# Optimization experiments

Measured on AMD Instinct MI355X. Metric: run time of the kernel, lower is better.

The kernel has to match this reference:

```python
import jax, jax.numpy as jnp
import numpy as np

EPS = 1e-06  # slot-attention renorm epsilon
LN_EPS = 1e-05  # torch LayerNorm default
NUM_ITERS = 3


def layernorm(x, w, b):
    m = jnp.mean(x, axis=-1, keepdims=True)
    v = jnp.mean((x - m) ** 2, axis=-1, keepdims=True)
    return (x - m) * jax.lax.rsqrt(v + LN_EPS) * w + b


def setup_inputs() -> dict:
    key = jax.random.key(0)
    ks = jax.random.split(key, 16)
    B, N, D = 32, 4096, 512
    S, NS, H = 128, 8, 256
    def lin(k, out_f, in_f):
        return jax.random.normal(k, (out_f, in_f), jnp.float32) * (1.0 / np.sqrt(in_f))
    return {
        "inputs": jax.random.normal(ks[0], (B, N, D), jnp.float32),
        "slots_init": jax.random.normal(ks[1], (B, NS, S), jnp.float32),
        "ln_in_w": jnp.ones((D,), jnp.float32), "ln_in_b": jnp.zeros((D,), jnp.float32),
        "ln_slot_w": jnp.ones((S,), jnp.float32), "ln_slot_b": jnp.zeros((S,), jnp.float32),
        "ln_mlp_w": jnp.ones((S,), jnp.float32), "ln_mlp_b": jnp.zeros((S,), jnp.float32),
        "Wq": lin(ks[2], S, S), "Wk": lin(ks[3], S, D), "Wv": lin(ks[4], S, D),
        "gru_Wih": lin(ks[5], 3 * S, S), "gru_Whh": lin(ks[6], 3 * S, S),
        "gru_bih": jnp.zeros((3 * S,), jnp.float32), "gru_bhh": jnp.zeros((3 * S,), jnp.float32),
        "mlp_W1": lin(ks[7], H, S), "mlp_b1": jnp.zeros((H,), jnp.float32),
        "mlp_W2": lin(ks[8], S, H), "mlp_b2": jnp.zeros((S,), jnp.float32),
        "slots_mu": jax.random.normal(ks[9], (1, 1, S), jnp.float32) * 0.1,
        "slots_log_sigma": jax.random.normal(ks[10], (1, 1, S), jnp.float32) * 0.1,
    }


def gru_cell(x, h, Wih, Whh, bih, bhh):
    # PyTorch GRUCell math. x, h: [BS, S]
    S = h.shape[-1]
    gi = x @ Wih.T + bih
    gh = h @ Whh.T + bhh
    i_r, i_z, i_n = gi[:, :S], gi[:, S:2 * S], gi[:, 2 * S:]
    h_r, h_z, h_n = gh[:, :S], gh[:, S:2 * S], gh[:, 2 * S:]
    r = jax.nn.sigmoid(i_r + h_r)
    z = jax.nn.sigmoid(i_z + h_z)
    n = jnp.tanh(i_n + r * h_n)
    return (1.0 - z) * n + z * h


def reference(inputs, slots_init, ln_in_w, ln_in_b, ln_slot_w, ln_slot_b, ln_mlp_w, ln_mlp_b,
              Wq, Wk, Wv, gru_Wih, gru_Whh, gru_bih, gru_bhh,
              mlp_W1, mlp_b1, mlp_W2, mlp_b2, slots_mu, slots_log_sigma):
    B, N, D = inputs.shape
    NS, S = slots_init.shape[1], slots_init.shape[2]
    x = layernorm(inputs, ln_in_w, ln_in_b)
    k = jnp.einsum('bnd,sd->bns', x, Wk)  # [B,N,S]
    v = jnp.einsum('bnd,sd->bns', x, Wv)
    slots = slots_mu + jnp.exp(slots_log_sigma) * slots_init  # [B,NS,S]
    scale = S ** (-0.5)
    for _ in range(NUM_ITERS):
        slots_prev = slots
        q = jnp.einsum('bmd,sd->bms', layernorm(slots, ln_slot_w, ln_slot_b), Wq)  # [B,NS,S]
        attn_logits = scale * jnp.einsum('bns,bms->bnm', k, q)  # [B,N,NS]
        attn = jax.nn.softmax(attn_logits, axis=-1) + EPS
        attn = attn / jnp.sum(attn, axis=1, keepdims=True)  # normalize over inputs
        updates = jnp.einsum('bnm,bns->bms', attn, v)  # [B,NS,S]
        h = gru_cell(updates.reshape(B * NS, S), slots_prev.reshape(B * NS, S),
                     gru_Wih, gru_Whh, gru_bih, gru_bhh).reshape(B, NS, S)
        mlp_out = jnp.maximum(layernorm(h, ln_mlp_w, ln_mlp_b) @ mlp_W1.T + mlp_b1, 0.0) @ mlp_W2.T + mlp_b2
        slots = h + mlp_out
    return slots
```

## Files before the change

### kernel.cpp

```cpp
#include <hip/hip_runtime.h>

typedef __bf16 v8bf __attribute__((ext_vector_type(8)));
typedef __bf16 v4bf __attribute__((ext_vector_type(4)));
typedef float  v4f  __attribute__((ext_vector_type(4)));
typedef unsigned short u16;

#define LN_EPS_F 1e-5f
#define ATTN_EPS 1e-6f

static constexpr int Bsz = 32;
static constexpr int Nn  = 4096;
static constexpr int Dd  = 512;
static constexpr int Ss  = 128;
static constexpr int NSs = 8;
static constexpr int Hh  = 256;
static constexpr int MROWS = Bsz * Nn;

__device__ __forceinline__ void load_lds16(const void* g, void* l) {
    __builtin_amdgcn_global_load_lds(
        (const __attribute__((address_space(1))) void*)g,
        (__attribute__((address_space(3))) void*)l, 16, 0, 0);
}

__global__ __launch_bounds__(256) void k_prep(const float* __restrict__ Wk, const float* __restrict__ Wv,
                                              const float* __restrict__ ln_in_w, const float* __restrict__ ln_in_b,
                                              const float* __restrict__ slots_init, const float* __restrict__ mu,
                                              const float* __restrict__ lsig,
                                              u16* __restrict__ Wkvp, float* __restrict__ cb,
                                              float* __restrict__ Scol, float* __restrict__ slots) {
    const int bid = blockIdx.x;
    const int t = threadIdx.x;
    if (bid < 512) {
        int idx = bid * 256 + t;
        int n = idx >> 9, d = idx & 511;
        float w = (n < Ss) ? Wk[n * Dd + d] : Wv[(n - Ss) * Dd + d];
        w *= ln_in_w[d];
        __bf16 bv = (__bf16)w;
        Wkvp[idx] = __builtin_bit_cast(u16, bv);
    } else if (bid < 640) {
        int idx = (bid - 512) * 256 + t;
        int sidx = idx & (Ss - 1);
        slots[idx] = mu[sidx] + expf(lsig[sidx]) * slots_init[idx];
    } else {
        const float* wrow = (t < Ss) ? (Wk + t * Dd) : (Wv + (t - Ss) * Dd);
        float accb = 0.f, accs = 0.f;
        for (int d = 0; d < Dd; ++d) {
            float w  = wrow[d];
            float wb = (float)(__bf16)(w * ln_in_w[d]);
            accs += wb;
            accb += ln_in_b[d] * w;
        }
        cb[t]   = accb;
        Scol[t] = accs;
    }
}

__global__ __launch_bounds__(256) void k_kvgemm(const float* __restrict__ X,
                                                const u16* __restrict__ Wkvp,
                                                const float* __restrict__ cb,
                                                const float* __restrict__ Scol,
                                                u16* __restrict__ kv) {
    __shared__ __bf16 As[64][72];
    __shared__ __bf16 Bs[256 * 64];
    __shared__ float2 stats_sh[64];
    const int t    = threadIdx.x;
    const int lane = t & 63;
    const int wid  = t >> 6;
    const size_t m0 = (size_t)blockIdx.x * 64;

    const int ar  = t >> 2;
    const int ac0 = (t & 3) * 16;
    const float* xrow = X + (m0 + ar) * Dd;

    const int sub  = lane >> 3;
    const int scol = ((lane & 7) ^ sub) * 8;
    const u16* bsrc = Wkvp + (size_t)(wid * 64 + sub) * Dd + scol;

    const v4f vzero = {0.f, 0.f, 0.f, 0.f};
    v4f acc[4][4];
#pragma unroll
    for (int i = 0; i < 4; ++i)
#pragma unroll
        for (int j = 0; j < 4; ++j) acc[i][j] = vzero;

    const int g  = lane >> 4;
    const int lr = lane & 15;
    float s1 = 0.f, s2 = 0.f;

    for (int kb = 0; kb < 8; ++kb) {
#pragma unroll
        for (int p = 0; p < 8; ++p)
            load_lds16(bsrc + (size_t)p * 8 * Dd + kb * 64,
                       &Bs[(wid * 64 + p * 8) * 64]);
#pragma unroll
        for (int j = 0; j < 4; ++j) {
            float4 xv = *reinterpret_cast<const float4*>(xrow + kb * 64 + ac0 + j * 4);
            s1 += xv.x + xv.y + xv.z + xv.w;
            s2 += xv.x * xv.x + xv.y * xv.y + xv.z * xv.z + xv.w * xv.w;
            v4bf wv;
            wv[0] = (__bf16)xv.x; wv[1] = (__bf16)xv.y;
            wv[2] = (__bf16)xv.z; wv[3] = (__bf16)xv.w;
            *reinterpret_cast<v4bf*>(&As[ar][ac0 + j * 4]) = wv;
        }
        __syncthreads();
#pragma unroll
        for (int ks = 0; ks < 2; ++ks) {
            v8bf a[4], b[4];
#pragma unroll
            for (int mi = 0; mi < 4; ++mi)
                a[mi] = *reinterpret_cast<const v8bf*>(&As[mi * 16 + lr][ks * 32 + g * 8]);
#pragma unroll
            for (int ni = 0; ni < 4; ++ni) {
                int r = wid * 64 + ni * 16 + lr;
                b[ni] = *reinterpret_cast<const v8bf*>(
                    &Bs[r * 64 + ((ks * 32 + g * 8) ^ ((lr & 7) * 8))]);
            }
#pragma unroll
            for (int mi = 0; mi < 4; ++mi)
#pragma unroll
                for (int ni = 0; ni < 4; ++ni)
                    acc[mi][ni] = __builtin_amdgcn_mfma_f32_16x16x32_bf16(a[mi], b[ni], acc[mi][ni], 0, 0, 0);
        }
        __syncthreads();
    }
    s1 += __shfl_xor(s1, 1); s1 += __shfl_xor(s1, 2);
    s2 += __shfl_xor(s2, 1); s2 += __shfl_xor(s2, 2);
    if ((t & 3) == 0) {
        float m = s1 * (1.f / Dd);
        float v = s2 * (1.f / Dd) - m * m;
        stats_sh[ar] = make_float2(m, rsqrtf(v + LN_EPS_F));
    }
    __syncthreads();
    float Sn[4], cbv[4];
#pragma unroll
    for (int ni = 0; ni < 4; ++ni) {
        int ng = wid * 64 + ni * 16 + lr;
        Sn[ni]  = Scol[ng];
        cbv[ni] = cb[ng];
    }
#pragma unroll
    for (int mi = 0; mi < 4; ++mi)
#pragma unroll
        for (int j = 0; j < 4; ++j) {
            float2 st = stats_sh[mi * 16 + g * 4 + j];
            size_t mg = m0 + mi * 16 + g * 4 + j;
#pragma unroll
            for (int ni = 0; ni < 4; ++ni) {
                int ng = wid * 64 + ni * 16 + lr;
                float val = st.y * (acc[mi][ni][j] - st.x * Sn[ni]) + cbv[ni];
                __bf16 bv = (__bf16)val;
                kv[mg * 256 + ng] = __builtin_bit_cast(u16, bv);
            }
        }
}

__global__ __launch_bounds__(128) void k_q(const float* __restrict__ slots,
                                           const float* __restrict__ lnw, const float* __restrict__ lnb,
                                           const float* __restrict__ Wq, float* __restrict__ q) {
    __shared__ float xs[128];
    __shared__ float red[4];
    const int t = threadIdx.x;
    const int bm = blockIdx.x;
    float x = slots[bm * 128 + t];
    float s = x, s2 = x * x;
#pragma unroll
    for (int off = 32; off > 0; off >>= 1) { s += __shfl_xor(s, off); s2 += __shfl_xor(s2, off); }
    const int wid = t >> 6, lane = t & 63;
    if (lane == 0) { red[wid * 2] = s; red[wid * 2 + 1] = s2; }
    __syncthreads();
    float S1 = red[0] + red[2], S2 = red[1] + red[3];
    float m = S1 * (1.f / 128.f);
    float rstd = rsqrtf(S2 * (1.f / 128.f) - m * m + LN_EPS_F);
    xs[t] = (x - m) * rstd * lnw[t] + lnb[t];
    __syncthreads();
    const float* wr = Wq + (size_t)t * 128;
    float acc = 0.f;
#pragma unroll 8
    for (int d = 0; d < 128; d += 4) {
        float4 w = *reinterpret_cast<const float4*>(wr + d);
        acc += w.x * xs[d] + w.y * xs[d + 1] + w.z * xs[d + 2] + w.w * xs[d + 3];
    }
    q[bm * 128 + t] = acc * 0.08838834764831845f;
}

__global__ __launch_bounds__(256) void k_attnupd(const u16* __restrict__ kv, const float* __restrict__ q,
                                                 float* __restrict__ upd_part, float* __restrict__ colsum_part) {
    __shared__ float qs[8 * 128];
    __shared__ float at[128][8];
    __shared__ __bf16 vt[128][128];
    __shared__ float colpart[4][8];
    const int b  = blockIdx.y;
    const int ch = blockIdx.x;
    const int t  = threadIdx.x;
    const int lane = t & 63, wv = t >> 6;
    *reinterpret_cast<float4*>(&qs[t * 4]) = *reinterpret_cast<const float4*>(&q[b * 1024 + t * 4]);
    __syncthreads();
    {
        const int rsub = lane >> 4;
        const int csub = (lane & 15) * 8;
#pragma unroll
        for (int p = 0; p < 8; ++p) {
            int row = wv * 32 + p * 4;
            const u16* src = kv + ((size_t)(b * Nn + ch * 128 + row + rsub)) * 256 + 128 + csub;
            load_lds16(src, &vt[row][0]);
        }
    }
    const int nl   = t >> 1;
    const int half = t & 1;
    const u16* krow = kv + ((size_t)(b * Nn + ch * 128 + nl)) * 256 + half * 64;
    float acc[8] = {0.f, 0.f, 0.f, 0.f, 0.f, 0.f, 0.f, 0.f};
#pragma unroll
    for (int c = 0; c < 8; ++c) {
        v8bf kvv = *reinterpret_cast<const v8bf*>(krow + c * 8);
        float kf[8];
#pragma unroll
        for (int j = 0; j < 8; ++j) kf[j] = (float)kvv[j];
#pragma unroll
        for (int m = 0; m < 8; ++m) {
            const float* qrow = &qs[m * 128 + half * 64 + c * 8];
            float aa = 0.f;
#pragma unroll
            for (int j = 0; j < 8; ++j) aa += kf[j] * qrow[j];
            acc[m] += aa;
        }
    }
#pragma unroll
    for (int m = 0; m < 8; ++m) acc[m] += __shfl_xor(acc[m], 1);
    float mx = acc[0];
#pragma unroll
    for (int m = 1; m < 8; ++m) mx = fmaxf(mx, acc[m]);
    float e[8]; float ssum = 0.f;
#pragma unroll
    for (int m = 0; m < 8; ++m) { e[m] = __expf(acc[m] - mx); ssum += e[m]; }
    float inv = 1.0f / ssum;
    float a8[8];
#pragma unroll
    for (int m = 0; m < 8; ++m) a8[m] = e[m] * inv + ATTN_EPS;
    *reinterpret_cast<float4*>(&at[nl][half * 4]) =
        make_float4(a8[half * 4], a8[half * 4 + 1], a8[half * 4 + 2], a8[half * 4 + 3]);
#pragma unroll
    for (int m = 0; m < 8; ++m) {
        float v = a8[m];
#pragma unroll
        for (int off = 32; off > 0; off >>= 1) v += __shfl_xor(v, off);
        if (lane == 0) colpart[wv][m] = v * 0.5f;
    }
    __syncthreads();
    const int m2 = t >> 5;
    const int s0 = (t & 31) * 4;
    float a0 = 0.f, a1 = 0.f, a2 = 0.f, a3 = 0.f;
#pragma unroll 4
    for (int n = 0; n < 128; ++n) {
        float a = at[n][m2];
        v4bf vvv = *reinterpret_cast<const v4bf*>(&vt[n][s0]);
        a0 += a * (float)vvv[0];
        a1 += a * (float)vvv[1];
        a2 += a * (float)vvv[2];
        a3 += a * (float)vvv[3];
    }
    *reinterpret_cast<float4*>(upd_part + ((size_t)(b * 32 + ch) * 8 + m2) * 128 + s0) =
        make_float4(a0, a1, a2, a3);
    if (t < 8)
        colsum_part[(b * 32 + ch) * 8 + t] =
            colpart[0][t] + colpart[1][t] + colpart[2][t] + colpart[3][t];
}

__global__ __launch_bounds__(128) void k_finishq(const float* __restrict__ upd_part,
                                                 const float* __restrict__ colsum_part,
                                                 const float* __restrict__ slots_in,
                                                 const float* __restrict__ Wih, const float* __restrict__ Whh,
                                                 const float* __restrict__ bih, const float* __restrict__ bhh,
                                                 const float* __restrict__ lnw, const float* __restrict__ lnb,
                                                 const float* __restrict__ W1, const float* __restrict__ b1,
                                                 const float* __restrict__ W2, const float* __restrict__ b2,
                                                 const float* __restrict__ lnsw, const float* __restrict__ lnsb,
                                                 const float* __restrict__ Wq,
                                                 float* __restrict__ slots_out, float* __restrict__ qout) {
    __shared__ float us[128], sp[128], hnorm[128], act[256];
    __shared__ float red[4];
    __shared__ float csum_sh;
    const int t  = threadIdx.x;
    const int bm = blockIdx.x;
    const int b = bm >> 3, m = bm & 7;
    if (t < 64) {
        float v = (t < 32) ? colsum_part[(b * 32 + t) * 8 + m] : 0.f;
#pragma unroll
        for (int off = 32; off > 0; off >>= 1) v += __shfl_xor(v, off);
        if (t == 0) csum_sh = v;
    }
    float u = 0.f;
    for (int chk = 0; chk < 32; ++chk)
        u += upd_part[((size_t)(b * 32 + chk) * 8 + m) * 128 + t];
    float h0 = slots_in[bm * 128 + t];
    sp[t] = h0;
    __syncthreads();
    u *= (1.0f / csum_sh);
    us[t] = u;
    __syncthreads();
    float gir = bih[t], giz = bih[Ss + t], gin = bih[2 * Ss + t];
    float ghr = bhh[t], ghz = bhh[Ss + t], ghn = bhh[2 * Ss + t];
#pragma unroll 4
    for (int d = 0; d < Ss; d += 4) {
        float u0 = us[d], u1 = us[d + 1], u2 = us[d + 2], u3 = us[d + 3];
        float p0 = sp[d], p1 = sp[d + 1], p2 = sp[d + 2], p3 = sp[d + 3];
        float4 w;
        w = *reinterpret_cast<const float4*>(Wih + (size_t)t * Ss + d);
        gir += w.x * u0 + w.y * u1 + w.z * u2 + w.w * u3;
        w = *reinterpret_cast<const float4*>(Wih + (size_t)(Ss + t) * Ss + d);
        giz += w.x * u0 + w.y * u1 + w.z * u2 + w.w * u3;
        w = *reinterpret_cast<const float4*>(Wih + (size_t)(2 * Ss + t) * Ss + d);
        gin += w.x * u0 + w.y * u1 + w.z * u2 + w.w * u3;
        w = *reinterpret_cast<const float4*>(Whh + (size_t)t * Ss + d);
        ghr += w.x * p0 + w.y * p1 + w.z * p2 + w.w * p3;
        w = *reinterpret_cast<const float4*>(Whh + (size_t)(Ss + t) * Ss + d);
        ghz += w.x * p0 + w.y * p1 + w.z * p2 + w.w * p3;
        w = *reinterpret_cast<const float4*>(Whh + (size_t)(2 * Ss + t) * Ss + d);
        ghn += w.x * p0 + w.y * p1 + w.z * p2 + w.w * p3;
    }
    float r  = 1.f / (1.f + __expf(-(gir + ghr)));
    float z  = 1.f / (1.f + __expf(-(giz + ghz)));
    float nn = tanhf(gin + r * ghn);
    float h  = (1.f - z) * nn + z * h0;
    float s = h, s2 = h * h;
#pragma unroll
    for (int off = 32; off > 0; off >>= 1) { s += __shfl_xor(s, off); s2 += __shfl_xor(s2, off); }
    const int lane = t & 63, w2 = t >> 6;
    if (lane == 0) { red[w2 * 2] = s; red[w2 * 2 + 1] = s2; }
    __syncthreads();
    float S1 = red[0] + red[2], S2 = red[1] + red[3];
    float mean = S1 * (1.f / Ss);
    float rstd = rsqrtf(S2 * (1.f / Ss) - mean * mean + LN_EPS_F);
    hnorm[t] = (h - mean) * rstd * lnw[t] + lnb[t];
    __syncthreads();
    float a1 = b1[t], a2 = b1[Ss + t];
#pragma unroll 4
    for (int d = 0; d < Ss; d += 4) {
        float h0_ = hnorm[d], h1_ = hnorm[d + 1], h2_ = hnorm[d + 2], h3_ = hnorm[d + 3];
        float4 w1v = *reinterpret_cast<const float4*>(W1 + (size_t)t * Ss + d);
        float4 w2v = *reinterpret_cast<const float4*>(W1 + (size_t)(Ss + t) * Ss + d);
        a1 += w1v.x * h0_ + w1v.y * h1_ + w1v.z * h2_ + w1v.w * h3_;
        a2 += w2v.x * h0_ + w2v.y * h1_ + w2v.z * h2_ + w2v.w * h3_;
    }
    act[t] = fmaxf(a1, 0.f);
    act[Ss + t] = fmaxf(a2, 0.f);
    __syncthreads();
    float o = b2[t];
#pragma unroll 4
    for (int j = 0; j < Hh; j += 4) {
        float4 wv = *reinterpret_cast<const float4*>(W2 + (size_t)t * Hh + j);
        o += wv.x * act[j] + wv.y * act[j + 1] + wv.z * act[j + 2] + wv.w * act[j + 3];
    }
    float snew = h + o;
    slots_out[bm * 128 + t] = snew;
    float ss1 = snew, ss2 = snew * snew;
#pragma unroll
    for (int off = 32; off > 0; off >>= 1) { ss1 += __shfl_xor(ss1, off); ss2 += __shfl_xor(ss2, off); }
    if (lane == 0) { red[w2 * 2] = ss1; red[w2 * 2 + 1] = ss2; }
    __syncthreads();
    float T1 = red[0] + red[2], T2 = red[1] + red[3];
    float m2 = T1 * (1.f / Ss);
    float rstd2 = rsqrtf(T2 * (1.f / Ss) - m2 * m2 + LN_EPS_F);
    hnorm[t] = (snew - m2) * rstd2 * lnsw[t] + lnsb[t];
    __syncthreads();
    const float* wr = Wq + (size_t)t * 128;
    float qa = 0.f;
#pragma unroll 8
    for (int d = 0; d < 128; d += 4) {
        float4 w = *reinterpret_cast<const float4*>(wr + d);
        qa += w.x * hnorm[d] + w.y * hnorm[d + 1] + w.z * hnorm[d + 2] + w.w * hnorm[d + 3];
    }
    qout[bm * 128 + t] = qa * 0.08838834764831845f;
}

extern "C" void kernel_launch(void* const* d_in, const int* in_sizes, int n_in,
                              void* d_out, int out_size, void* d_ws, size_t ws_size,
                              hipStream_t stream) {
    const float* X          = (const float*)d_in[0];
    const float* slots_init = (const float*)d_in[1];
    const float* ln_in_w    = (const float*)d_in[2];
    const float* ln_in_b    = (const float*)d_in[3];
    const float* ln_slot_w  = (const float*)d_in[4];
    const float* ln_slot_b  = (const float*)d_in[5];
    const float* ln_mlp_w   = (const float*)d_in[6];
    const float* ln_mlp_b   = (const float*)d_in[7];
    const float* Wq         = (const float*)d_in[8];
    const float* Wk         = (const float*)d_in[9];
    const float* Wv         = (const float*)d_in[10];
    const float* gWih       = (const float*)d_in[11];
    const float* gWhh       = (const float*)d_in[12];
    const float* gbih       = (const float*)d_in[13];
    const float* gbhh       = (const float*)d_in[14];
    const float* W1         = (const float*)d_in[15];
    const float* b1         = (const float*)d_in[16];
    const float* W2         = (const float*)d_in[17];
    const float* b2         = (const float*)d_in[18];
    const float* mu         = (const float*)d_in[19];
    const float* lsig       = (const float*)d_in[20];

    char* p = (char*)d_ws;
    u16*    Wkvp        = (u16*)p;    p += (size_t)256 * 512 * sizeof(u16);
    float*  cb          = (float*)p;  p += 256 * sizeof(float);
    float*  Scol        = (float*)p;  p += 256 * sizeof(float);
    float*  slots       = (float*)p;  p += 32 * 8 * 128 * sizeof(float);
    float*  qbuf        = (float*)p;  p += 32 * 8 * 128 * sizeof(float);
    float*  colsum_part = (float*)p;  p += 32 * 32 * 8 * sizeof(float);
    float*  upd_part    = (float*)p;  p += (size_t)32 * 32 * 8 * 128 * sizeof(float);
    u16*    kv          = (u16*)p;    p += (size_t)MROWS * 256 * sizeof(u16);

    k_prep<<<641, 256, 0, stream>>>(Wk, Wv, ln_in_w, ln_in_b, slots_init, mu, lsig,
                                    Wkvp, cb, Scol, slots);
    k_kvgemm<<<MROWS / 64, 256, 0, stream>>>(X, Wkvp, cb, Scol, kv);
    k_q<<<256, 128, 0, stream>>>(slots, ln_slot_w, ln_slot_b, Wq, qbuf);

    for (int it = 0; it < 3; ++it) {
        k_attnupd<<<dim3(32, 32), 256, 0, stream>>>(kv, qbuf, upd_part, colsum_part);
        k_finishq<<<256, 128, 0, stream>>>(upd_part, colsum_part, slots,
                                           gWih, gWhh, gbih, gbhh,
                                           ln_mlp_w, ln_mlp_b, W1, b1, W2, b2,
                                           ln_slot_w, ln_slot_b, Wq,
                                           (it == 2) ? (float*)d_out : slots, qbuf);
    }
}
```

Baseline: 308.3 us.

## Double-buffer kvgemm weight tiles, parallelize prep reduction, widen finishq to 256 threads

The k_kvgemm main loop now double-buffers the weight tiles in LDS and prefetches the next X chunk into registers. It replaces __syncthreads with explicit waitcnt/barrier sequences so global loads overlap the MFMA work. The serial per-thread column-sum loop in k_prep is spread across 8 blocks, with wave-parallel float4 loads and shuffle reductions. k_finishq moves to 256 threads and splits each GEMV's reduction dimension across two halves, at the cost of more LDS partials and barriers.

```diff
diff --git a/kernel.cpp b/kernel.cpp
--- a/kernel.cpp
+++ b/kernel.cpp
@@ -42,16 +42,32 @@
         int sidx = idx & (Ss - 1);
         slots[idx] = mu[sidx] + expf(lsig[sidx]) * slots_init[idx];
     } else {
-        const float* wrow = (t < Ss) ? (Wk + t * Dd) : (Wv + (t - Ss) * Dd);
-        float accb = 0.f, accs = 0.f;
-        for (int d = 0; d < Dd; ++d) {
-            float w  = wrow[d];
-            float wb = (float)(__bf16)(w * ln_in_w[d]);
-            accs += wb;
-            accb += ln_in_b[d] * w;
-        }
-        cb[t]   = accb;
-        Scol[t] = accs;
+        const int wid = t >> 6, lane = t & 63;
+        const int rowbase = (bid - 640) * 32 + wid * 8;
+        const int d0 = lane * 8;
+        float4 lw0 = *reinterpret_cast<const float4*>(ln_in_w + d0);
+        float4 lw1 = *reinterpret_cast<const float4*>(ln_in_w + d0 + 4);
+        float4 lb0 = *reinterpret_cast<const float4*>(ln_in_b + d0);
+        float4 lb1 = *reinterpret_cast<const float4*>(ln_in_b + d0 + 4);
+        for (int rr = 0; rr < 8; ++rr) {
+            int row = rowbase + rr;
+            const float* wrow = (row < Ss) ? (Wk + (size_t)row * Dd)
+                                           : (Wv + (size_t)(row - Ss) * Dd);
+            float4 w0 = *reinterpret_cast<const float4*>(wrow + d0);
+            float4 w1 = *reinterpret_cast<const float4*>(wrow + d0 + 4);
+            float accb = lb0.x*w0.x + lb0.y*w0.y + lb0.z*w0.z + lb0.w*w0.w
+                       + lb1.x*w1.x + lb1.y*w1.y + lb1.z*w1.z + lb1.w*w1.w;
+            float accs = (float)(__bf16)(w0.x*lw0.x) + (float)(__bf16)(w0.y*lw0.y)
+                       + (float)(__bf16)(w0.z*lw0.z) + (float)(__bf16)(w0.w*lw0.w)
+                       + (float)(__bf16)(w1.x*lw1.x) + (float)(__bf16)(w1.y*lw1.y)
+                       + (float)(__bf16)(w1.z*lw1.z) + (float)(__bf16)(w1.w*lw1.w);
+#pragma unroll
+            for (int off = 32; off > 0; off >>= 1) {
+                accb += __shfl_xor(accb, off);
+                accs += __shfl_xor(accs, off);
+            }
+            if (lane == 0) { cb[row] = accb; Scol[row] = accs; }
+        }
     }
 }
 
@@ -61,7 +77,7 @@
                                                 const float* __restrict__ Scol,
                                                 u16* __restrict__ kv) {
     __shared__ __bf16 As[64][72];
-    __shared__ __bf16 Bs[256 * 64];
+    __shared__ __bf16 Bs[2][256 * 64];
     __shared__ float2 stats_sh[64];
     const int t    = threadIdx.x;
     const int lane = t & 63;
@@ -87,14 +103,22 @@
     const int lr = lane & 15;
     float s1 = 0.f, s2 = 0.f;
 
+    float4 a_pre[4];
+#pragma unroll
+    for (int j = 0; j < 4; ++j)
+        a_pre[j] = *reinterpret_cast<const float4*>(xrow + ac0 + j * 4);
+#pragma unroll
+    for (int p = 0; p < 8; ++p)
+        load_lds16(bsrc + (size_t)p * 8 * Dd, &Bs[0][(wid * 64 + p * 8) * 64]);
+#pragma unroll
+    for (int p = 0; p < 8; ++p)
+        load_lds16(bsrc + (size_t)p * 8 * Dd + 64, &Bs[1][(wid * 64 + p * 8) * 64]);
+
+#pragma unroll
     for (int kb = 0; kb < 8; ++kb) {
 #pragma unroll
-        for (int p = 0; p < 8; ++p)
-            load_lds16(bsrc + (size_t)p * 8 * Dd + kb * 64,
-                       &Bs[(wid * 64 + p * 8) * 64]);
-#pragma unroll
         for (int j = 0; j < 4; ++j) {
-            float4 xv = *reinterpret_cast<const float4*>(xrow + kb * 64 + ac0 + j * 4);
+            float4 xv = a_pre[j];
             s1 += xv.x + xv.y + xv.z + xv.w;
             s2 += xv.x * xv.x + xv.y * xv.y + xv.z * xv.z + xv.w * xv.w;
             v4bf wv;
@@ -102,26 +126,43 @@
             wv[2] = (__bf16)xv.z; wv[3] = (__bf16)xv.w;
             *reinterpret_cast<v4bf*>(&As[ar][ac0 + j * 4]) = wv;
         }
-        __syncthreads();
-#pragma unroll
-        for (int ks = 0; ks < 2; ++ks) {
-            v8bf a[4], b[4];
-#pragma unroll
-            for (int mi = 0; mi < 4; ++mi)
-                a[mi] = *reinterpret_cast<const v8bf*>(&As[mi * 16 + lr][ks * 32 + g * 8]);
-#pragma unroll
-            for (int ni = 0; ni < 4; ++ni) {
-                int r = wid * 64 + ni * 16 + lr;
-                b[ni] = *reinterpret_cast<const v8bf*>(
-                    &Bs[r * 64 + ((ks * 32 + g * 8) ^ ((lr & 7) * 8))]);
+        if (kb < 7) {
+#pragma unroll
+            for (int j = 0; j < 4; ++j)
+                a_pre[j] = *reinterpret_cast<const float4*>(xrow + (kb + 1) * 64 + ac0 + j * 4);
+        }
+        if (kb < 7)
+            asm volatile("s_waitcnt vmcnt(12) lgkmcnt(0)\ns_barrier" ::: "memory");
+        else
+            asm volatile("s_waitcnt vmcnt(0) lgkmcnt(0)\ns_barrier" ::: "memory");
+        {
+            const __bf16* bbase = &Bs[kb & 1][0];
+#pragma unroll
+            for (int ks = 0; ks < 2; ++ks) {
+                v8bf a[4], bfr[4];
+#pragma unroll
+                for (int mi = 0; mi < 4; ++mi)
+                    a[mi] = *reinterpret_cast<const v8bf*>(&As[mi * 16 + lr][ks * 32 + g * 8]);
+#pragma unroll
+                for (int ni = 0; ni < 4; ++ni) {
+                    int r = wid * 64 + ni * 16 + lr;
+                    bfr[ni] = *reinterpret_cast<const v8bf*>(
+                        &bbase[r * 64 + ((ks * 32 + g * 8) ^ ((lr & 7) * 8))]);
+                }
+#pragma unroll
+                for (int mi = 0; mi < 4; ++mi)
+#pragma unroll
+                    for (int ni = 0; ni < 4; ++ni)
+                        acc[mi][ni] = __builtin_amdgcn_mfma_f32_16x16x32_bf16(a[mi], bfr[ni], acc[mi][ni], 0, 0, 0);
             }
-#pragma unroll
-            for (int mi = 0; mi < 4; ++mi)
-#pragma unroll
-                for (int ni = 0; ni < 4; ++ni)
-                    acc[mi][ni] = __builtin_amdgcn_mfma_f32_16x16x32_bf16(a[mi], b[ni], acc[mi][ni], 0, 0, 0);
-        }
-        __syncthreads();
+        }
+        asm volatile("s_barrier" ::: "memory");
+        if (kb < 6) {
+#pragma unroll
+            for (int p = 0; p < 8; ++p)
+                load_lds16(bsrc + (size_t)p * 8 * Dd + (kb + 2) * 64,
+                           &Bs[kb & 1][(wid * 64 + p * 8) * 64]);
+        }
     }
     s1 += __shfl_xor(s1, 1); s1 += __shfl_xor(s1, 2);
     s2 += __shfl_xor(s2, 1); s2 += __shfl_xor(s2, 2);
@@ -265,7 +306,7 @@
             colpart[0][t] + colpart[1][t] + colpart[2][t] + colpart[3][t];
 }
 
-__global__ __launch_bounds__(128) void k_finishq(const float* __restrict__ upd_part,
+__global__ __launch_bounds__(256) void k_finishq(const float* __restrict__ upd_part,
                                                  const float* __restrict__ colsum_part,
                                                  const float* __restrict__ slots_in,
                                                  const float* __restrict__ Wih, const float* __restrict__ Whh,
@@ -276,11 +317,16 @@
                                                  const float* __restrict__ lnsw, const float* __restrict__ lnsb,
                                                  const float* __restrict__ Wq,
                                                  float* __restrict__ slots_out, float* __restrict__ qout) {
-    __shared__ float us[128], sp[128], hnorm[128], act[256];
+    __shared__ float us[128], sp[128], hnorm[128], qsrc[128], act[256];
+    __shared__ float upart[2][128];
+    __shared__ float gpart[2][6][128];
+    __shared__ float p2[2][128];
+    __shared__ float qpart[2][128];
     __shared__ float red[4];
     __shared__ float csum_sh;
-    const int t  = threadIdx.x;
-    const int bm = blockIdx.x;
+    const int t   = threadIdx.x;
+    const int tid = t & 127, half = t >> 7;
+    const int bm  = blockIdx.x;
     const int b = bm >> 3, m = bm & 7;
     if (t < 64) {
         float v = (t < 32) ? colsum_part[(b * 32 + t) * 8 + m] : 0.f;
@@ -289,87 +335,117 @@
         if (t == 0) csum_sh = v;
     }
     float u = 0.f;
-    for (int chk = 0; chk < 32; ++chk)
-        u += upd_part[((size_t)(b * 32 + chk) * 8 + m) * 128 + t];
-    float h0 = slots_in[bm * 128 + t];
-    sp[t] = h0;
-    __syncthreads();
-    u *= (1.0f / csum_sh);
-    us[t] = u;
-    __syncthreads();
-    float gir = bih[t], giz = bih[Ss + t], gin = bih[2 * Ss + t];
-    float ghr = bhh[t], ghz = bhh[Ss + t], ghn = bhh[2 * Ss + t];
-#pragma unroll 4
-    for (int d = 0; d < Ss; d += 4) {
-        float u0 = us[d], u1 = us[d + 1], u2 = us[d + 2], u3 = us[d + 3];
-        float p0 = sp[d], p1 = sp[d + 1], p2 = sp[d + 2], p3 = sp[d + 3];
-        float4 w;
-        w = *reinterpret_cast<const float4*>(Wih + (size_t)t * Ss + d);
-        gir += w.x * u0 + w.y * u1 + w.z * u2 + w.w * u3;
-        w = *reinterpret_cast<const float4*>(Wih + (size_t)(Ss + t) * Ss + d);
-        giz += w.x * u0 + w.y * u1 + w.z * u2 + w.w * u3;
-        w = *reinterpret_cast<const float4*>(Wih + (size_t)(2 * Ss + t) * Ss + d);
-        gin += w.x * u0 + w.y * u1 + w.z * u2 + w.w * u3;
-        w = *reinterpret_cast<const float4*>(Whh + (size_t)t * Ss + d);
-        ghr += w.x * p0 + w.y * p1 + w.z * p2 + w.w * p3;
-        w = *reinterpret_cast<const float4*>(Whh + (size_t)(Ss + t) * Ss + d);
-        ghz += w.x * p0 + w.y * p1 + w.z * p2 + w.w * p3;
-        w = *reinterpret_cast<const float4*>(Whh + (size_t)(2 * Ss + t) * Ss + d);
-        ghn += w.x * p0 + w.y * p1 + w.z * p2 + w.w * p3;
-    }
+#pragma unroll 4
+    for (int chk = half * 16; chk < half * 16 + 16; ++chk)
+        u += upd_part[((size_t)(b * 32 + chk) * 8 + m) * 128 + tid];
+    upart[half][tid] = u;
+    if (half == 0) sp[tid] = slots_in[bm * 128 + tid];
+    __syncthreads();
+    if (half == 0) us[tid] = (upart[0][tid] + upart[1][tid]) * (1.f / csum_sh);
+    __syncthreads();
+    {
+        const int d0g = half * 64;
+        float a_r = 0.f, a_z = 0.f, a_n = 0.f, b_r = 0.f, b_z = 0.f, b_n = 0.f;
+        const float* Wr = Wih + (size_t)tid * 128 + d0g;
+        const float* Wz = Wih + (size_t)(128 + tid) * 128 + d0g;
+        const float* Wn = Wih + (size_t)(256 + tid) * 128 + d0g;
+        const float* Vr = Whh + (size_t)tid * 128 + d0g;
+        const float* Vz = Whh + (size_t)(128 + tid) * 128 + d0g;
+        const float* Vn = Whh + (size_t)(256 + tid) * 128 + d0g;
+#pragma unroll 4
+        for (int d = 0; d < 64; d += 4) {
+            float u0 = us[d0g + d], u1 = us[d0g + d + 1], u2 = us[d0g + d + 2], u3 = us[d0g + d + 3];
+            float p0 = sp[d0g + d], p1 = sp[d0g + d + 1], p2_ = sp[d0g + d + 2], p3 = sp[d0g + d + 3];
+            float4 w;
+            w = *reinterpret_cast<const float4*>(Wr + d); a_r += w.x*u0 + w.y*u1 + w.z*u2 + w.w*u3;
+            w = *reinterpret_cast<const float4*>(Wz + d); a_z += w.x*u0 + w.y*u1 + w.z*u2 + w.w*u3;
+            w = *reinterpret_cast<const float4*>(Wn + d); a_n += w.x*u0 + w.y*u1 + w.z*u2 + w.w*u3;
+            w = *reinterpret_cast<const float4*>(Vr + d); b_r += w.x*p0 + w.y*p1 + w.z*p2_ + w.w*p3;
+            w = *reinterpret_cast<const float4*>(Vz + d); b_z += w.x*p0 + w.y*p1 + w.z*p2_ + w.w*p3;
+            w = *reinterpret_cast<const float4*>(Vn + d); b_n += w.x*p0 + w.y*p1 + w.z*p2_ + w.w*p3;
+        }
+        gpart[half][0][tid] = a_r; gpart[half][1][tid] = a_z; gpart[half][2][tid] = a_n;
+        gpart[half][3][tid] = b_r; gpart[half][4][tid] = b_z; gpart[half][5][tid] = b_n;
+    }
+    __syncthreads();
+    float gir = bih[tid]       + gpart[0][0][tid] + gpart[1][0][tid];
+    float giz = bih[128 + tid] + gpart[0][1][tid] + gpart[1][1][tid];
+    float gin = bih[256 + tid] + gpart[0][2][tid] + gpart[1][2][tid];
+    float ghr = bhh[tid]       + gpart[0][3][tid] + gpart[1][3][tid];
+    float ghz = bhh[128 + tid] + gpart[0][4][tid] + gpart[1][4][tid];
+    float ghn = bhh[256 + tid] + gpart[0][5][tid] + gpart[1][5][tid];
+    float h0 = sp[tid];
     float r  = 1.f / (1.f + __expf(-(gir + ghr)));
     float z  = 1.f / (1.f + __expf(-(giz + ghz)));
     float nn = tanhf(gin + r * ghn);
     float h  = (1.f - z) * nn + z * h0;
-    float s = h, s2 = h * h;
-#pragma unroll
-    for (int off = 32; off > 0; off >>= 1) { s += __shfl_xor(s, off); s2 += __shfl_xor(s2, off); }
-    const int lane = t & 63, w2 = t >> 6;
-    if (lane == 0) { red[w2 * 2] = s; red[w2 * 2 + 1] = s2; }
-    __syncthreads();
-    float S1 = red[0] + red[2], S2 = red[1] + red[3];
-    float mean = S1 * (1.f / Ss);
-    float rstd = rsqrtf(S2 * (1.f / Ss) - mean * mean + LN_EPS_F);
-    hnorm[t] = (h - mean) * rstd * lnw[t] + lnb[t];
-    __syncthreads();
-    float a1 = b1[t], a2 = b1[Ss + t];
-#pragma unroll 4
-    for (int d = 0; d < Ss; d += 4) {
-        float h0_ = hnorm[d], h1_ = hnorm[d + 1], h2_ = hnorm[d + 2], h3_ = hnorm[d + 3];
-        float4 w1v = *reinterpret_cast<const float4*>(W1 + (size_t)t * Ss + d);
-        float4 w2v = *reinterpret_cast<const float4*>(W1 + (size_t)(Ss + t) * Ss + d);
-        a1 += w1v.x * h0_ + w1v.y * h1_ + w1v.z * h2_ + w1v.w * h3_;
-        a2 += w2v.x * h0_ + w2v.y * h1_ + w2v.z * h2_ + w2v.w * h3_;
-    }
-    act[t] = fmaxf(a1, 0.f);
-    act[Ss + t] = fmaxf(a2, 0.f);
-    __syncthreads();
-    float o = b2[t];
-#pragma unroll 4
-    for (int j = 0; j < Hh; j += 4) {
-        float4 wv = *reinterpret_cast<const float4*>(W2 + (size_t)t * Hh + j);
-        o += wv.x * act[j] + wv.y * act[j + 1] + wv.z * act[j + 2] + wv.w * act[j + 3];
-    }
-    float snew = h + o;
-    slots_out[bm * 128 + t] = snew;
-    float ss1 = snew, ss2 = snew * snew;
-#pragma unroll
-    for (int off = 32; off > 0; off >>= 1) { ss1 += __shfl_xor(ss1, off); ss2 += __shfl_xor(ss2, off); }
-    if (lane == 0) { red[w2 * 2] = ss1; red[w2 * 2 + 1] = ss2; }
-    __syncthreads();
-    float T1 = red[0] + red[2], T2 = red[1] + red[3];
-    float m2 = T1 * (1.f / Ss);
-    float rstd2 = rsqrtf(T2 * (1.f / Ss) - m2 * m2 + LN_EPS_F);
-    hnorm[t] = (snew - m2) * rstd2 * lnsw[t] + lnsb[t];
-    __syncthreads();
-    const float* wr = Wq + (size_t)t * 128;
-    float qa = 0.f;
-#pragma unroll 8
-    for (int d = 0; d < 128; d += 4) {
-        float4 w = *reinterpret_cast<const float4*>(wr + d);
-        qa += w.x * hnorm[d] + w.y * hnorm[d + 1] + w.z * hnorm[d + 2] + w.w * hnorm[d + 3];
-    }
-    qout[bm * 128 + t] = qa * 0.08838834764831845f;
+    if (half == 0) {
+        float s = h, s2 = h * h;
+#pragma unroll
+        for (int off = 32; off > 0; off >>= 1) { s += __shfl_xor(s, off); s2 += __shfl_xor(s2, off); }
+        if ((t & 63) == 0) { red[(tid >> 6) * 2] = s; red[(tid >> 6) * 2 + 1] = s2; }
+    }
+    __syncthreads();
+    {
+        float S1 = red[0] + red[2], S2 = red[1] + red[3];
+        float mean = S1 * (1.f / Ss);
+        float rstd = rsqrtf(S2 * (1.f / Ss) - mean * mean + LN_EPS_F);
+        if (half == 0) hnorm[tid] = (h - mean) * rstd * lnw[tid] + lnb[tid];
+    }
+    __syncthreads();
+    {
+        float a = b1[t];
+        const float* w1r = W1 + (size_t)t * 128;
+#pragma unroll 4
+        for (int d = 0; d < 128; d += 4) {
+            float4 w = *reinterpret_cast<const float4*>(w1r + d);
+            a += w.x * hnorm[d] + w.y * hnorm[d + 1] + w.z * hnorm[d + 2] + w.w * hnorm[d + 3];
+        }
+        act[t] = fmaxf(a, 0.f);
+    }
+    __syncthreads();
+    {
+        float o = 0.f;
+        const int j0 = half * 128;
+        const float* w2r = W2 + (size_t)tid * 256 + j0;
+#pragma unroll 4
+        for (int j = 0; j < 128; j += 4) {
+            float4 w = *reinterpret_cast<const float4*>(w2r + j);
+            o += w.x * act[j0 + j] + w.y * act[j0 + j + 1] + w.z * act[j0 + j + 2] + w.w * act[j0 + j + 3];
+        }
+        p2[half][tid] = o;
+    }
+    __syncthreads();
+    float snew = h + b2[tid] + p2[0][tid] + p2[1][tid];
+    if (half == 0) slots_out[bm * 128 + tid] = snew;
+    if (half == 0) {
+        float s = snew, s2 = snew * snew;
+#pragma unroll
+        for (int off = 32; off > 0; off >>= 1) { s += __shfl_xor(s, off); s2 += __shfl_xor(s2, off); }
+        if ((t & 63) == 0) { red[(tid >> 6) * 2] = s; red[(tid >> 6) * 2 + 1] = s2; }
+    }
+    __syncthreads();
+    {
+        float T1 = red[0] + red[2], T2 = red[1] + red[3];
+        float m2 = T1 * (1.f / Ss);
+        float rstd2 = rsqrtf(T2 * (1.f / Ss) - m2 * m2 + LN_EPS_F);
+        if (half == 0) qsrc[tid] = (snew - m2) * rstd2 * lnsw[tid] + lnsb[tid];
+    }
+    __syncthreads();
+    {
+        float qa = 0.f;
+        const int d0g = half * 64;
+        const float* wr = Wq + (size_t)tid * 128 + d0g;
+#pragma unroll 4
+        for (int d = 0; d < 64; d += 4) {
+            float4 w = *reinterpret_cast<const float4*>(wr + d);
+            qa += w.x * qsrc[d0g + d] + w.y * qsrc[d0g + d + 1] + w.z * qsrc[d0g + d + 2] + w.w * qsrc[d0g + d + 3];
+        }
+        qpart[half][tid] = qa;
+    }
+    __syncthreads();
+    if (half == 0)
+        qout[bm * 128 + tid] = (qpart[0][tid] + qpart[1][tid]) * 0.08838834764831845f;
 }
 
 extern "C" void kernel_launch(void* const* d_in, const int* in_sizes, int n_in,
@@ -407,14 +483,14 @@
     float*  upd_part    = (float*)p;  p += (size_t)32 * 32 * 8 * 128 * sizeof(float);
     u16*    kv          = (u16*)p;    p += (size_t)MROWS * 256 * sizeof(u16);
 
-    k_prep<<<641, 256, 0, stream>>>(Wk, Wv, ln_in_w, ln_in_b, slots_init, mu, lsig,
+    k_prep<<<648, 256, 0, stream>>>(Wk, Wv, ln_in_w, ln_in_b, slots_init, mu, lsig,
                                     Wkvp, cb, Scol, slots);
     k_kvgemm<<<MROWS / 64, 256, 0, stream>>>(X, Wkvp, cb, Scol, kv);
     k_q<<<256, 128, 0, stream>>>(slots, ln_slot_w, ln_slot_b, Wq, qbuf);
 
     for (int it = 0; it < 3; ++it) {
         k_attnupd<<<dim3(32, 32), 256, 0, stream>>>(kv, qbuf, upd_part, colsum_part);
-        k_finishq<<<256, 128, 0, stream>>>(upd_part, colsum_part, slots,
+        k_finishq<<<256, 256, 0, stream>>>(upd_part, colsum_part, slots,
                                            gWih, gWhh, gbih, gbhh,
                                            ln_mlp_w, ln_mlp_b, W1, b1, W2, b2,
                                            ln_slot_w, ln_slot_b, Wq,
```

Measured after the change: 306.6 us, median of 2. Within noise of the previous version (-0.5%).
